# Optimization experiments

Hardware: AMD Instinct MI355X
Metric: run time of the kernel (lower is better)

Reference implementation:

```python
import jax, jax.numpy as jnp
import numpy as np

D = 16      # core_size
R = 8       # rank
SIZE = D ** 3  # 4096, nr_cores = 3


def setup_inputs() -> dict:
    key = jax.random.key(0)
    k = jax.random.split(key, 5)
    core_std = np.sqrt(2.0 / D).astype(np.float32)  # kaiming_normal over (-1, d, d)
    x = jax.random.normal(k[0], (8, 1024, SIZE), dtype=jnp.float32)
    core0 = core_std * jax.random.normal(k[1], (D, D, D, D, R, 1), dtype=jnp.float32)
    core1 = core_std * jax.random.normal(k[2], (D, D, D, D, R, R), dtype=jnp.float32)
    core2 = core_std * jax.random.normal(k[3], (D, D, D, D, 1, R), dtype=jnp.float32)
    bias = np.sqrt(1.0 / SIZE).astype(np.float32) * jax.random.uniform(
        k[4], (SIZE,), dtype=jnp.float32, minval=-1.0, maxval=1.0)
    return {"x": x, "core0": core0, "core1": core1, "core2": core2, "bias": bias}


def to_matrix(core0, core1, core2):
    # Faithful translation of BTT.to_matrix for nr_cores=3.
    # G starts as core0: (d,d,d,d,r,1)
    # step idx=0 (core1): j=d, i=d^2
    c1 = core1.reshape(D, D * D, D, R, R)          # jixcb
    g = core0.reshape(D, D * D, D, R, 1)           # jiyba
    G = jnp.einsum('jixcb,jiyba->jiyxca', c1, g)   # (d, d^2, d, d, r, 1)
    # step idx=1 (core2): j=d^2, i=d
    c2 = core2.reshape(D * D, D, D, 1, R)          # jixcb
    g = G.reshape(D * D, D, D * D, R, 1)           # jiyba
    G = jnp.einsum('jixcb,jiyba->jiyxca', c2, g)   # (d^2, d, d^2, d, 1, 1)
    return G.reshape(SIZE, SIZE)


def reference(x, core0, core1, core2, bias):
    G = to_matrix(core0, core1, core2)
    out = x.reshape(-1, SIZE) @ G + bias
    return out.reshape(x.shape)
```

## Files before the change

kernel.cpp:

```cpp
#include <hip/hip_runtime.h>
#include <stdint.h>

typedef unsigned short u16;
typedef short bf16x8 __attribute__((ext_vector_type(8)));
typedef float f32x4 __attribute__((ext_vector_type(4)));
typedef u16 u16x4 __attribute__((ext_vector_type(4)));

__device__ __forceinline__ u16 f2bf(float f) {
    union { float f; unsigned int i; } v; v.f = f;
    unsigned int x = v.i;
    return (u16)((x + 0x7FFFu + ((x >> 16) & 1u)) >> 16);
}

__device__ __forceinline__ void async_load16(const u16* g, u16* lds) {
    __builtin_amdgcn_global_load_lds(
        (const __attribute__((address_space(1))) unsigned int*)g,
        (__attribute__((address_space(3))) unsigned int*)lds,
        16, 0, 0);
}

__global__ void build_gt(const float* __restrict__ c0, const float* __restrict__ c1,
                         const float* __restrict__ c2, u16* __restrict__ Gt) {
    const int y1  = blockIdx.x >> 4;
    const int x1  = blockIdx.x & 15;
    const int r   = blockIdx.y * 256 + threadIdx.x;

    float a0[8];
    {
        f32x4 v0 = *(const f32x4*)(c0 + ((size_t)r * 16 + y1) * 8);
        f32x4 v1 = *(const f32x4*)(c0 + ((size_t)r * 16 + y1) * 8 + 4);
        #pragma unroll
        for (int b = 0; b < 4; ++b) { a0[b] = v0[b]; a0[4 + b] = v1[b]; }
    }
    float t[8];
    const float* c1row = c1 + ((size_t)r * 16 + x1) * 64;
    #pragma unroll
    for (int c = 0; c < 8; ++c) {
        f32x4 v0 = *(const f32x4*)(c1row + c * 8);
        f32x4 v1 = *(const f32x4*)(c1row + c * 8 + 4);
        float s = 0.f;
        #pragma unroll
        for (int b = 0; b < 4; ++b) s += v0[b] * a0[b] + v1[b] * a0[4 + b];
        t[c] = s;
    }
    const float* c2row = c2 + (size_t)r * 128;
    #pragma unroll
    for (int x2 = 0; x2 < 16; ++x2) {
        f32x4 v0 = *(const f32x4*)(c2row + x2 * 8);
        f32x4 v1 = *(const f32x4*)(c2row + x2 * 8 + 4);
        float s = 0.f;
        #pragma unroll
        for (int c = 0; c < 4; ++c) s += v0[c] * t[c] + v1[c] * t[4 + c];
        Gt[((size_t)(blockIdx.x * 16 + x2)) * 4096 + r] = f2bf(s);
    }
}

__global__ void conv_x(const f32x4* __restrict__ x, u16* __restrict__ xb, int n4) {
    for (int i = blockIdx.x * 256 + threadIdx.x; i < n4; i += gridDim.x * 256) {
        f32x4 v = x[i];
        u16x4 o;
        #pragma unroll
        for (int j = 0; j < 4; ++j) o[j] = f2bf(v[j]);
        *(u16x4*)(xb + 4 * (size_t)i) = o;
    }
}

__global__ __launch_bounds__(512, 2)
void gemm_8ph(const u16* __restrict__ Xb, const u16* __restrict__ Gt,
              const float* __restrict__ bias, float* __restrict__ out) {
    constexpr int K = 4096, N = 4096, NT = 64;
    extern __shared__ u16 lds[];

    const int tid  = threadIdx.x;
    const int lane = tid & 63;
    const int w    = tid >> 6;
    const int wmi  = w >> 2;
    const int wni  = w & 3;
    const int lr   = lane & 15;
    const int lq   = lane >> 4;
    const int xr   = lr & 7;

    const int m0 = blockIdx.y * 256;
    const int n0 = blockIdx.x * 256;

    const int r0 = tid >> 3;
    const int s0 = (tid & 7) ^ (r0 & 7);
    const int r1 = 64 + r0;
    const int s1 = ((512 + tid) & 7) ^ (r1 & 7);
    const size_t aoff0 = (size_t)(m0 + r0) * K + s0 * 8;
    const size_t aoff1 = (size_t)(m0 + r1) * K + s1 * 8;
    const size_t boff0 = (size_t)(n0 + r0) * K + s0 * 8;
    const size_t boff1 = (size_t)(n0 + r1) * K + s1 * 8;
    const int ldsw0 = (tid & ~63) * 8;
    const int ldsw1 = 4096 + (tid & ~63) * 8;

    const int aoffL = (wmi * 16 + lr) * 64;
    const int boffL = 16384 + (wni * 16 + lr) * 64;
    const int slot0 = (lq ^ xr) * 8;
    const int slot1 = ((4 + lq) ^ xr) * 8;

    f32x4 acc[8][4] = {};
    bf16x8 a[4][2], b2[2][2];

    auto stageA = [&](int b, int h, int t) {
        const u16* s = Xb + (size_t)h * (128 * K) + (size_t)t * 64;
        u16* d = lds + b * 32768 + h * 8192;
        async_load16(s + aoff0, d + ldsw0);
        async_load16(s + aoff1, d + ldsw1);
    };
    auto stageB = [&](int b, int h, int t) {
        const u16* s = Gt + (size_t)h * (128 * K) + (size_t)t * 64;
        u16* d = lds + b * 32768 + 16384 + h * 8192;
        async_load16(s + boff0, d + ldsw0);
        async_load16(s + boff1, d + ldsw1);
    };
    auto loadA = [&](int b, int h) {
        const u16* p = lds + b * 32768 + h * 8192 + aoffL;
        #pragma unroll
        for (int li = 0; li < 4; ++li) {
            a[li][0] = *(const bf16x8*)(p + li * 2048 + slot0);
            a[li][1] = *(const bf16x8*)(p + li * 2048 + slot1);
        }
    };
    auto loadB = [&](int b, int h) {
        const u16* p = lds + b * 32768 + h * 8192 + boffL;
        #pragma unroll
        for (int lj = 0; lj < 2; ++lj) {
            b2[lj][0] = *(const bf16x8*)(p + lj * 4096 + slot0);
            b2[lj][1] = *(const bf16x8*)(p + lj * 4096 + slot1);
        }
    };
    auto mfmaQ = [&](int mh, int nh) {
        #pragma unroll
        for (int li = 0; li < 4; ++li)
            #pragma unroll
            for (int lj = 0; lj < 2; ++lj) {
                f32x4 c = acc[mh * 4 + li][nh * 2 + lj];
                c = __builtin_amdgcn_mfma_f32_16x16x32_bf16(a[li][0], b2[lj][0], c, 0, 0, 0);
                c = __builtin_amdgcn_mfma_f32_16x16x32_bf16(a[li][1], b2[lj][1], c, 0, 0, 0);
                acc[mh * 4 + li][nh * 2 + lj] = c;
            }
    };

    stageA(0, 0, 0); stageB(0, 0, 0);
    stageA(0, 1, 0); stageB(0, 1, 0);
    stageA(1, 0, 1); stageB(1, 0, 1);
    asm volatile("s_waitcnt vmcnt(8)" ::: "memory");
    __builtin_amdgcn_s_barrier();

    for (int T = 0; T < NT; ++T) {
        const int bc = T & 1, bn = bc ^ 1;
        const int t1 = (T + 1) & (NT - 1);
        const int t2 = (T + 2) & (NT - 1);

        loadA(bc, 0); loadB(bc, 0);
        stageA(bn, 1, t1);
        __builtin_amdgcn_s_barrier();
        asm volatile("s_waitcnt lgkmcnt(0)" ::: "memory");
        __builtin_amdgcn_s_setprio(1);
        mfmaQ(0, 0);
        __builtin_amdgcn_s_setprio(0);
        asm volatile("s_waitcnt vmcnt(6)" ::: "memory");
        __builtin_amdgcn_s_barrier();

        loadB(bc, 1);
        stageB(bn, 1, t1);
        __builtin_amdgcn_s_barrier();
        asm volatile("s_waitcnt lgkmcnt(0)" ::: "memory");
        __builtin_amdgcn_s_setprio(1);
        mfmaQ(0, 1);
        __builtin_amdgcn_s_setprio(0);
        __builtin_amdgcn_s_barrier();

        loadA(bc, 1); loadB(bc, 0);
        stageA(bc, 0, t2);
        __builtin_amdgcn_s_barrier();
        asm volatile("s_waitcnt lgkmcnt(0)" ::: "memory");
        __builtin_amdgcn_s_setprio(1);
        mfmaQ(1, 0);
        __builtin_amdgcn_s_setprio(0);
        __builtin_amdgcn_s_barrier();

        loadB(bc, 1);
        stageB(bc, 0, t2);
        __builtin_amdgcn_s_barrier();
        asm volatile("s_waitcnt lgkmcnt(0)" ::: "memory");
        __builtin_amdgcn_s_setprio(1);
        mfmaQ(1, 1);
        __builtin_amdgcn_s_setprio(0);
        asm volatile("s_waitcnt vmcnt(8)" ::: "memory");
        __builtin_amdgcn_s_barrier();
    }
    asm volatile("s_waitcnt vmcnt(0)" ::: "memory");

    #pragma unroll
    for (int j = 0; j < 4; ++j) {
        const int n = n0 + (j * 4 + wni) * 16 + lr;
        const float bv = bias[n];
        #pragma unroll
        for (int i = 0; i < 8; ++i) {
            const int mb = m0 + (2 * i + wmi) * 16 + lq * 4;
            #pragma unroll
            for (int r = 0; r < 4; ++r)
                out[(size_t)(mb + r) * N + n] = acc[i][j][r] + bv;
        }
    }
}

#define TM 128
#define TN 128
#define BK 32

__global__ void gemm_bt_f32(const float* __restrict__ Xf, const u16* __restrict__ Gt,
                            const float* __restrict__ bias, float* __restrict__ out) {
    constexpr int K = 4096, N = 4096;
    __shared__ __attribute__((aligned(16))) u16 As[TM * BK];
    __shared__ __attribute__((aligned(16))) u16 Bs[TN * BK];

    const int tid  = threadIdx.x;
    const int lane = tid & 63;
    const int w    = tid >> 6;
    const int m0   = blockIdx.y * TM;
    const int n0   = blockIdx.x * TN;
    const int wm   = (w >> 1) * 64;
    const int wn   = (w & 1) * 64;
    const int lr   = lane & 15;
    const int lk   = (lane >> 4) * 8;

    f32x4 acc[4][4] = {};

    const int srow   = tid >> 2;
    const int schunk = (tid & 3) * 8;
    const u16* grow0 = Gt + (size_t)(n0 + srow) * K + schunk;
    const u16* grow1 = Gt + (size_t)(n0 + 64 + srow) * K + schunk;
    u16* ldsB0 = &Bs[(tid & ~63) * 8];
    u16* ldsB1 = &Bs[(256 + (tid & ~63)) * 8];

    const float* xsrc = Xf + (size_t)(m0 + (tid >> 1)) * K + (tid & 1) * 16;
    u16* adst = &As[(tid >> 1) * BK + (tid & 1) * 16];

    for (int k0 = 0; k0 < K; k0 += BK) {
        __syncthreads();
        {
            f32x4 v0 = ((const f32x4*)(xsrc + k0))[0];
            f32x4 v1 = ((const f32x4*)(xsrc + k0))[1];
            f32x4 v2 = ((const f32x4*)(xsrc + k0))[2];
            f32x4 v3 = ((const f32x4*)(xsrc + k0))[3];
            bf16x8 w0, w1;
            #pragma unroll
            for (int j = 0; j < 4; ++j) {
                w0[j]     = (short)f2bf(v0[j]);
                w0[4 + j] = (short)f2bf(v1[j]);
                w1[j]     = (short)f2bf(v2[j]);
                w1[4 + j] = (short)f2bf(v3[j]);
            }
            *(bf16x8*)adst = w0;
            *(bf16x8*)(adst + 8) = w1;
        }
        async_load16(grow0 + k0, ldsB0);
        async_load16(grow1 + k0, ldsB1);
        __syncthreads();

        bf16x8 af[4], bg[4];
        #pragma unroll
        for (int i = 0; i < 4; ++i) {
            af[i] = *(const bf16x8*)(&As[(wm + i * 16 + lr) * BK + lk]);
            bg[i] = *(const bf16x8*)(&Bs[(wn + i * 16 + lr) * BK + lk]);
        }
        #pragma unroll
        for (int mt = 0; mt < 4; ++mt)
            #pragma unroll
            for (int nt = 0; nt < 4; ++nt)
                acc[mt][nt] = __builtin_amdgcn_mfma_f32_16x16x32_bf16(
                    af[mt], bg[nt], acc[mt][nt], 0, 0, 0);
    }

    #pragma unroll
    for (int nt = 0; nt < 4; ++nt) {
        const int n = n0 + wn + nt * 16 + lr;
        const float bv = bias[n];
        #pragma unroll
        for (int mt = 0; mt < 4; ++mt) {
            const int mbase = m0 + wm + mt * 16 + (lane >> 4) * 4;
            #pragma unroll
            for (int r = 0; r < 4; ++r) {
                out[(size_t)(mbase + r) * N + n] = acc[mt][nt][r] + bv;
            }
        }
    }
}

extern "C" void kernel_launch(void* const* d_in, const int* in_sizes, int n_in,
                              void* d_out, int out_size, void* d_ws, size_t ws_size,
                              hipStream_t stream) {
    const float* x    = (const float*)d_in[0];
    const float* c0   = (const float*)d_in[1];
    const float* c1   = (const float*)d_in[2];
    const float* c2   = (const float*)d_in[3];
    const float* bias = (const float*)d_in[4];
    float* out = (float*)d_out;

    const size_t GT_BYTES = (size_t)4096 * 4096 * sizeof(u16);
    const size_t XB_BYTES = (size_t)8192 * 4096 * sizeof(u16);
    u16* Gt = (u16*)d_ws;

    build_gt<<<dim3(256, 16), 256, 0, stream>>>(c0, c1, c2, Gt);

    if (ws_size >= GT_BYTES + XB_BYTES) {
        u16* Xb = (u16*)((char*)d_ws + GT_BYTES);
        conv_x<<<8192, 256, 0, stream>>>((const f32x4*)x, Xb, 8192 * 4096 / 4);
        static int attr_done = 0;
        if (!attr_done) {
            hipFuncSetAttribute(reinterpret_cast<const void*>(gemm_8ph),
                                hipFuncAttributeMaxDynamicSharedMemorySize, 131072);
            attr_done = 1;
        }
        gemm_8ph<<<dim3(16, 32), 512, 131072, stream>>>(Xb, Gt, bias, out);
    } else {
        gemm_bt_f32<<<dim3(32, 64), 256, 0, stream>>>(x, Gt, bias, out);
    }
}
```

Before: 565.5 us.

## Transpose TT cores for coalesced G build and keep both B fragment halves in registers

The cores are transposed into r-major layouts so the G-construction kernel can read them with coalesced f32x4 loads and produce four output columns per thread. The Xb region serves as scratch before conv_x overwrites it. In the GEMM, both halves of the B fragments are kept in separate registers, which removes two redundant LDS reloads and one lgkmcnt wait per iteration. The cost is three extra transpose launches and higher VGPR pressure in the GEMM.

```diff
diff --git a/kernel.cpp b/kernel.cpp
--- a/kernel.cpp
+++ b/kernel.cpp
@@ -17,6 +17,63 @@
         (const __attribute__((address_space(1))) unsigned int*)g,
         (__attribute__((address_space(3))) unsigned int*)lds,
         16, 0, 0);
+}
+
+__global__ void transpose_f32(const float* __restrict__ in, float* __restrict__ out,
+                              int Q) {
+    __shared__ float t[64][65];
+    const int r0 = blockIdx.y * 64;
+    const int q0 = blockIdx.x * 64;
+    const int tx = threadIdx.x & 63;
+    const int ty = threadIdx.x >> 6;
+    #pragma unroll
+    for (int k = 0; k < 16; ++k) {
+        const int row = k * 4 + ty;
+        t[row][tx] = in[(size_t)(r0 + row) * Q + q0 + tx];
+    }
+    __syncthreads();
+    #pragma unroll
+    for (int k = 0; k < 16; ++k) {
+        const int qrow = k * 4 + ty;
+        out[(size_t)(q0 + qrow) * 4096 + r0 + tx] = t[tx][qrow];
+    }
+}
+
+__global__ void build_gt_t(const float* __restrict__ c0t, const float* __restrict__ c1t,
+                           const float* __restrict__ c2t, u16* __restrict__ Gt) {
+    const int y1 = blockIdx.x >> 4;
+    const int x1 = blockIdx.x & 15;
+    const int r0 = blockIdx.y * 1024 + threadIdx.x * 4;
+
+    f32x4 a0[8];
+    #pragma unroll
+    for (int b = 0; b < 8; ++b)
+        a0[b] = *(const f32x4*)(c0t + (size_t)(y1 * 8 + b) * 4096 + r0);
+
+    f32x4 t[8];
+    #pragma unroll
+    for (int c = 0; c < 8; ++c) {
+        f32x4 s = {0.f, 0.f, 0.f, 0.f};
+        #pragma unroll
+        for (int b = 0; b < 8; ++b) {
+            f32x4 w = *(const f32x4*)(c1t + (size_t)(x1 * 64 + c * 8 + b) * 4096 + r0);
+            s += w * a0[b];
+        }
+        t[c] = s;
+    }
+    #pragma unroll
+    for (int x2 = 0; x2 < 16; ++x2) {
+        f32x4 s = {0.f, 0.f, 0.f, 0.f};
+        #pragma unroll
+        for (int c = 0; c < 8; ++c) {
+            f32x4 w = *(const f32x4*)(c2t + (size_t)(x2 * 8 + c) * 4096 + r0);
+            s += w * t[c];
+        }
+        u16x4 o;
+        #pragma unroll
+        for (int j = 0; j < 4; ++j) o[j] = f2bf(s[j]);
+        *(u16x4*)(Gt + (size_t)(blockIdx.x * 16 + x2) * 4096 + r0) = o;
+    }
 }
 
 __global__ void build_gt(const float* __restrict__ c0, const float* __restrict__ c1,
@@ -100,34 +157,35 @@
     const int slot1 = ((4 + lq) ^ xr) * 8;
 
     f32x4 acc[8][4] = {};
-    bf16x8 a[4][2], b2[2][2];
-
-    auto stageA = [&](int b, int h, int t) {
+    bf16x8 a[4][2];
+    bf16x8 bfr[2][2][2];
+
+    auto stageA = [&](int bb, int h, int t) {
         const u16* s = Xb + (size_t)h * (128 * K) + (size_t)t * 64;
-        u16* d = lds + b * 32768 + h * 8192;
+        u16* d = lds + bb * 32768 + h * 8192;
         async_load16(s + aoff0, d + ldsw0);
         async_load16(s + aoff1, d + ldsw1);
     };
-    auto stageB = [&](int b, int h, int t) {
+    auto stageB = [&](int bb, int h, int t) {
         const u16* s = Gt + (size_t)h * (128 * K) + (size_t)t * 64;
-        u16* d = lds + b * 32768 + 16384 + h * 8192;
+        u16* d = lds + bb * 32768 + 16384 + h * 8192;
         async_load16(s + boff0, d + ldsw0);
         async_load16(s + boff1, d + ldsw1);
     };
-    auto loadA = [&](int b, int h) {
-        const u16* p = lds + b * 32768 + h * 8192 + aoffL;
+    auto loadA = [&](int bb, int h) {
+        const u16* p = lds + bb * 32768 + h * 8192 + aoffL;
         #pragma unroll
         for (int li = 0; li < 4; ++li) {
             a[li][0] = *(const bf16x8*)(p + li * 2048 + slot0);
             a[li][1] = *(const bf16x8*)(p + li * 2048 + slot1);
         }
     };
-    auto loadB = [&](int b, int h) {
-        const u16* p = lds + b * 32768 + h * 8192 + boffL;
+    auto loadB = [&](int bb, int h) {
+        const u16* p = lds + bb * 32768 + h * 8192 + boffL;
         #pragma unroll
         for (int lj = 0; lj < 2; ++lj) {
-            b2[lj][0] = *(const bf16x8*)(p + lj * 4096 + slot0);
-            b2[lj][1] = *(const bf16x8*)(p + lj * 4096 + slot1);
+            bfr[h][lj][0] = *(const bf16x8*)(p + lj * 4096 + slot0);
+            bfr[h][lj][1] = *(const bf16x8*)(p + lj * 4096 + slot1);
         }
     };
     auto mfmaQ = [&](int mh, int nh) {
@@ -136,8 +194,8 @@
             #pragma unroll
             for (int lj = 0; lj < 2; ++lj) {
                 f32x4 c = acc[mh * 4 + li][nh * 2 + lj];
-                c = __builtin_amdgcn_mfma_f32_16x16x32_bf16(a[li][0], b2[lj][0], c, 0, 0, 0);
-                c = __builtin_amdgcn_mfma_f32_16x16x32_bf16(a[li][1], b2[lj][1], c, 0, 0, 0);
+                c = __builtin_amdgcn_mfma_f32_16x16x32_bf16(a[li][0], bfr[nh][lj][0], c, 0, 0, 0);
+                c = __builtin_amdgcn_mfma_f32_16x16x32_bf16(a[li][1], bfr[nh][lj][1], c, 0, 0, 0);
                 acc[mh * 4 + li][nh * 2 + lj] = c;
             }
     };
@@ -172,7 +230,7 @@
         __builtin_amdgcn_s_setprio(0);
         __builtin_amdgcn_s_barrier();
 
-        loadA(bc, 1); loadB(bc, 0);
+        loadA(bc, 1);
         stageA(bc, 0, t2);
         __builtin_amdgcn_s_barrier();
         asm volatile("s_waitcnt lgkmcnt(0)" ::: "memory");
@@ -181,10 +239,8 @@
         __builtin_amdgcn_s_setprio(0);
         __builtin_amdgcn_s_barrier();
 
-        loadB(bc, 1);
         stageB(bc, 0, t2);
         __builtin_amdgcn_s_barrier();
-        asm volatile("s_waitcnt lgkmcnt(0)" ::: "memory");
         __builtin_amdgcn_s_setprio(1);
         mfmaQ(1, 1);
         __builtin_amdgcn_s_setprio(0);
@@ -304,11 +360,20 @@
     const size_t XB_BYTES = (size_t)8192 * 4096 * sizeof(u16);
     u16* Gt = (u16*)d_ws;
 
-    build_gt<<<dim3(256, 16), 256, 0, stream>>>(c0, c1, c2, Gt);
-
     if (ws_size >= GT_BYTES + XB_BYTES) {
+        char* scratch = (char*)d_ws + GT_BYTES;
+        float* c1t = (float*)scratch;
+        float* c0t = (float*)(scratch + (size_t)16 * 1024 * 1024);
+        float* c2t = (float*)(scratch + (size_t)18 * 1024 * 1024);
+
+        transpose_f32<<<dim3(16, 64), 256, 0, stream>>>(c1, c1t, 1024);
+        transpose_f32<<<dim3(2, 64), 256, 0, stream>>>(c0, c0t, 128);
+        transpose_f32<<<dim3(2, 64), 256, 0, stream>>>(c2, c2t, 128);
+        build_gt_t<<<dim3(256, 4), 256, 0, stream>>>(c0t, c1t, c2t, Gt);
+
         u16* Xb = (u16*)((char*)d_ws + GT_BYTES);
         conv_x<<<8192, 256, 0, stream>>>((const f32x4*)x, Xb, 8192 * 4096 / 4);
+
         static int attr_done = 0;
         if (!attr_done) {
             hipFuncSetAttribute(reinterpret_cast<const void*>(gemm_8ph),
@@ -317,6 +382,7 @@
         }
         gemm_8ph<<<dim3(16, 32), 512, 131072, stream>>>(Xb, Gt, bias, out);
     } else {
+        build_gt<<<dim3(256, 16), 256, 0, stream>>>(c0, c1, c2, Gt);
         gemm_bt_f32<<<dim3(32, 64), 256, 0, stream>>>(x, Gt, bias, out);
     }
 }
```

After: 501.5 us. 1.13x faster.
